# Kernel tuning notes

Hardware: AMD Instinct MI355X
Metric: run time of the kernel (lower is better)

The kernel has to match this reference:

```python
import jax, jax.numpy as jnp
import numpy as np

EMBED_DIM = 1024
NUM_HEADS = 16
HEAD_DIM = EMBED_DIM // NUM_HEADS


def setup_inputs() -> dict:
    key = jax.random.key(0)
    ks = jax.random.split(key, 9)
    B, T, D = 2, 4096, EMBED_DIM
    scale = 1.0 / np.sqrt(D)
    x = jax.random.normal(ks[0], (B, T, D), dtype=jnp.float32)
    # nn.Linear weights stored as (out, in); we use (in, out) layout via transpose-free init
    Wq = jax.random.uniform(ks[1], (D, D), dtype=jnp.float32, minval=-scale, maxval=scale)
    Wk = jax.random.uniform(ks[2], (D, D), dtype=jnp.float32, minval=-scale, maxval=scale)
    Wv = jax.random.uniform(ks[3], (D, D), dtype=jnp.float32, minval=-scale, maxval=scale)
    Wo = jax.random.uniform(ks[4], (D, D), dtype=jnp.float32, minval=-scale, maxval=scale)
    bq = jax.random.uniform(ks[5], (D,), dtype=jnp.float32, minval=-scale, maxval=scale)
    bk = jax.random.uniform(ks[6], (D,), dtype=jnp.float32, minval=-scale, maxval=scale)
    bv = jax.random.uniform(ks[7], (D,), dtype=jnp.float32, minval=-scale, maxval=scale)
    bo = jax.random.uniform(ks[8], (D,), dtype=jnp.float32, minval=-scale, maxval=scale)
    return {"x": x, "Wq": Wq, "bq": bq, "Wk": Wk, "bk": bk,
            "Wv": Wv, "bv": bv, "Wo": Wo, "bo": bo}


def reference(x, Wq, bq, Wk, bk, Wv, bv, Wo, bo):
    B, T, D = x.shape
    H, Hd = NUM_HEADS, HEAD_DIM
    q = x @ Wq + bq  # [B,T,D]
    k = x @ Wk + bk
    v = x @ Wv + bv
    # [B,T,D] -> [B,H,T,Hd]
    q = q.reshape(B, T, H, Hd).transpose(0, 2, 1, 3)
    k = k.reshape(B, T, H, Hd).transpose(0, 2, 1, 3)
    v = v.reshape(B, T, H, Hd).transpose(0, 2, 1, 3)
    att = jnp.einsum('bhqd,bhkd->bhqk', q, k) / jnp.sqrt(jnp.float32(Hd))
    causal = jnp.tril(jnp.ones((T, T), dtype=bool))  # True = keep
    att = jnp.where(causal, att, -jnp.inf)
    att = jax.nn.softmax(att, axis=-1)
    out = jnp.einsum('bhqk,bhkd->bhqd', att, v)  # [B,H,T,Hd]
    out = out.transpose(0, 2, 1, 3).reshape(B, T, D)
    return out @ Wo + bo
```

## Files before the change

### kernel.cpp

```cpp
#include <hip/hip_runtime.h>
#include <hip/hip_bf16.h>
#include <math.h>

typedef __bf16 bf16;
typedef __attribute__((ext_vector_type(8))) __bf16 bf16x8;
typedef __attribute__((ext_vector_type(4))) __bf16 bf16x4;
typedef __attribute__((ext_vector_type(4))) short short4v;
typedef __attribute__((ext_vector_type(4))) float f32x4;

#define MFMA16(a,b,c)  __builtin_amdgcn_mfma_f32_16x16x32_bf16((a),(b),(c),0,0,0)
#define MFMAK16(a,b,c) __builtin_amdgcn_mfma_f32_16x16x16bf16_1k((a),(b),(c),0,0,0)

__device__ __forceinline__ void gload16(const void* gp, void* lp) {
  __builtin_amdgcn_global_load_lds(
      (const __attribute__((address_space(1))) void*)gp,
      (__attribute__((address_space(3))) void*)lp, 16, 0, 0);
}

__global__ __launch_bounds__(256) void cast_x(
    const float* __restrict__ x, bf16* __restrict__ xb)
{
  size_t i = ((size_t)blockIdx.x*256 + threadIdx.x) * 8;
  f32x4 a = *(const f32x4*)(x+i);
  f32x4 b = *(const f32x4*)(x+i+4);
  bf16x8 o;
  #pragma unroll
  for (int j=0;j<4;j++) { o[j] = (bf16)a[j]; o[4+j] = (bf16)b[j]; }
  *(bf16x8*)(xb+i) = o;
}

__global__ __launch_bounds__(1024) void tr_cast(
    const float* __restrict__ w0, const float* __restrict__ w1,
    const float* __restrict__ w2, bf16* __restrict__ dst)
{
  __shared__ bf16 tile[64][65];
  const float* src = (blockIdx.z==0)?w0:(blockIdx.z==1)?w1:w2;
  bf16* d = dst + (size_t)blockIdx.z * (1024*1024);
  int x = threadIdx.x, y = threadIdx.y;
  int tc = blockIdx.x, tr = blockIdx.y;
  #pragma unroll
  for (int i=0;i<4;i++) {
    int r = y + i*16;
    tile[r][x] = (bf16)src[(size_t)(tr*64+r)*1024 + tc*64 + x];
  }
  __syncthreads();
  #pragma unroll
  for (int i=0;i<4;i++) {
    int r = y + i*16;
    d[(size_t)(tc*64+r)*1024 + tr*64 + x] = tile[x][r];
  }
}

__global__ __launch_bounds__(256) void gemm_qkv(
    const bf16* __restrict__ A, const bf16* __restrict__ Bt,
    const float* __restrict__ bq, const float* __restrict__ bk, const float* __restrict__ bv,
    bf16* __restrict__ q, bf16* __restrict__ k, bf16* __restrict__ v,
    int M, int K)
{
  __shared__ __align__(16) bf16 As[128*32];
  __shared__ __align__(16) bf16 Bs[128*32];
  const int tid  = threadIdx.x;
  const int wave = tid >> 6;
  const int lane = tid & 63;
  const int l15  = lane & 15;
  const int quad = lane >> 4;
  const int m0 = blockIdx.y * 128;
  const int n0 = blockIdx.x * 128;
  const int wm = (wave >> 1) * 64;
  const int wn = (wave & 1) * 64;
  const int srow = lane >> 2;
  const int scol = (lane & 3) * 8;

  f32x4 acc[4][4];
  #pragma unroll
  for (int i=0;i<4;i++)
    #pragma unroll
    for (int j=0;j<4;j++)
      acc[i][j] = (f32x4){0.f,0.f,0.f,0.f};

  for (int k0 = 0; k0 < K; k0 += 32) {
    __syncthreads();
    #pragma unroll
    for (int p=0;p<2;p++) {
      int c = p*4 + wave;
      int row = c*16 + srow;
      gload16(A  + (size_t)(m0+row)*K + k0 + scol, As + c*512);
      gload16(Bt + (size_t)(n0+row)*K + k0 + scol, Bs + c*512);
    }
    __syncthreads();
    bf16x8 af[4], bfr[4];
    #pragma unroll
    for (int t=0;t<4;t++) {
      af[t]  = *(const bf16x8*)(As + (wm + t*16 + l15)*32 + quad*8);
      bfr[t] = *(const bf16x8*)(Bs + (wn + t*16 + l15)*32 + quad*8);
    }
    #pragma unroll
    for (int mt=0;mt<4;mt++)
      #pragma unroll
      for (int nt=0;nt<4;nt++)
        acc[mt][nt] = MFMA16(af[mt], bfr[nt], acc[mt][nt]);
  }

  const int mat = n0 >> 10;
  const float* bsel = (mat==0) ? bq : (mat==1) ? bk : bv;
  bf16*       osel  = (mat==0) ? q  : (mat==1) ? k  : v;
  const float qsc   = (mat==0) ? 0.1803368801f : 1.0f;
  #pragma unroll
  for (int nt=0;nt<4;nt++) {
    int col = n0 + wn + nt*16 + l15;
    int cw  = col & 1023;
    float bvv = bsel[cw];
    #pragma unroll
    for (int mt=0;mt<4;mt++) {
      int row = m0 + wm + mt*16 + quad*4;
      #pragma unroll
      for (int r=0;r<4;r++)
        osel[(size_t)(row + r)*1024 + cw] = (bf16)((acc[mt][nt][r] + bvv) * qsc);
    }
  }
}

__global__ __launch_bounds__(256) void gemm_out(
    const bf16* __restrict__ A, const bf16* __restrict__ Bt,
    const float* __restrict__ bias, float* __restrict__ C,
    int M, int N, int K)
{
  __shared__ __align__(16) bf16 As[128*32];
  __shared__ __align__(16) bf16 Bs[128*32];
  const int tid  = threadIdx.x;
  const int wave = tid >> 6;
  const int lane = tid & 63;
  const int l15  = lane & 15;
  const int quad = lane >> 4;
  const int m0 = blockIdx.y * 128;
  const int n0 = blockIdx.x * 128;
  const int wm = (wave >> 1) * 64;
  const int wn = (wave & 1) * 64;
  const int srow = lane >> 2;
  const int scol = (lane & 3) * 8;

  f32x4 acc[4][4];
  #pragma unroll
  for (int i=0;i<4;i++)
    #pragma unroll
    for (int j=0;j<4;j++)
      acc[i][j] = (f32x4){0.f,0.f,0.f,0.f};

  for (int k0 = 0; k0 < K; k0 += 32) {
    __syncthreads();
    #pragma unroll
    for (int p=0;p<2;p++) {
      int c = p*4 + wave;
      int row = c*16 + srow;
      gload16(A  + (size_t)(m0+row)*K + k0 + scol, As + c*512);
      gload16(Bt + (size_t)(n0+row)*K + k0 + scol, Bs + c*512);
    }
    __syncthreads();
    bf16x8 af[4], bfr[4];
    #pragma unroll
    for (int t=0;t<4;t++) {
      af[t]  = *(const bf16x8*)(As + (wm + t*16 + l15)*32 + quad*8);
      bfr[t] = *(const bf16x8*)(Bs + (wn + t*16 + l15)*32 + quad*8);
    }
    #pragma unroll
    for (int mt=0;mt<4;mt++)
      #pragma unroll
      for (int nt=0;nt<4;nt++)
        acc[mt][nt] = MFMA16(af[mt], bfr[nt], acc[mt][nt]);
  }

  #pragma unroll
  for (int nt=0;nt<4;nt++) {
    int col = n0 + wn + nt*16 + l15;
    float bvv = bias[col];
    #pragma unroll
    for (int mt=0;mt<4;mt++) {
      int row = m0 + wm + mt*16 + quad*4;
      #pragma unroll
      for (int r=0;r<4;r++)
        C[(size_t)(row + r)*N + col] = acc[mt][nt][r] + bvv;
    }
  }
}

__global__ __launch_bounds__(256, 5) void attn_fwd(
    const bf16* __restrict__ Q, const bf16* __restrict__ Kp,
    const bf16* __restrict__ V, bf16* __restrict__ O)
{
  __shared__ __align__(16) char KsB[2*8192];
  __shared__ __align__(16) char VtB[2*8192];

  const int tid  = threadIdx.x;
  const int w    = tid >> 6;
  const int lane = tid & 63;
  const int l15  = lane & 15;
  const int quad = lane >> 4;

  const int bid = blockIdx.x;
  const int qt  = 63 - (bid >> 5);
  const int bh  = bid & 31;
  const int h   = bh & 15;
  const int b   = bh >> 4;

  const size_t headoff = (size_t)h * 64;
  const size_t bbase   = (size_t)b * 4096;

  bf16x8 aq[2];
  {
    int row = qt*64 + w*16 + l15;
    const bf16* qp = Q + (bbase + row)*1024 + headoff + quad*8;
    aq[0] = *(const bf16x8*)(qp);
    aq[1] = *(const bf16x8*)(qp + 32);
  }

  short4v ones_s;
  {
    bf16x4 o1;
    #pragma unroll
    for (int j=0;j<4;j++) o1[j] = (bf16)1.0f;
    ones_s = __builtin_bit_cast(short4v, o1);
  }

  f32x4 acco[4];
  f32x4 accli;
  #pragma unroll
  for (int i=0;i<4;i++) acco[i] = (f32x4){0.f,0.f,0.f,0.f};
  accli = (f32x4){0.f,0.f,0.f,0.f};

  const int kt_row = tid >> 2;
  const int kswz   = (kt_row & 7) << 4;
  const int ks_w0  = kt_row*128 + (((tid & 3)*32)      ^ kswz);
  const int ks_w1  = kt_row*128 + (((tid & 3)*32 + 16) ^ kswz);
  const int vt_wbase = w*2048;
  const int vt_wlane = 2*lane;

  const int s7    = l15 & 7;
  const int ks_r0 = l15*128 + ((quad ^ (s7 & 3)) << 4) + ((s7 >> 2) << 6);
  const int ks_r1 = ks_r0 ^ 64;
  const int vt_rbase = l15*128 + ((quad ^ (l15 & 3)) << 3) + ((l15 >> 2) << 5);
  int vt_r[4];
  #pragma unroll
  for (int tt=0;tt<4;tt++) vt_r[tt] = vt_rbase ^ (tt << 5);

  {
    const bf16* kp = Kp + (bbase + kt_row)*1024 + headoff + (tid & 3)*16;
    bf16x8 k0 = *(const bf16x8*)(kp);
    bf16x8 k1 = *(const bf16x8*)(kp + 8);
    *(bf16x8*)(KsB + ks_w0) = k0;
    *(bf16x8*)(KsB + ks_w1) = k1;
    const bf16* vp = V + (bbase + lane)*1024 + headoff + w*16;
    bf16x8 v0 = *(const bf16x8*)(vp);
    bf16x8 v1 = *(const bf16x8*)(vp + 8);
    #pragma unroll
    for (int j=0;j<8;j++) {
      *(bf16*)(VtB + vt_wbase + j*128     + (vt_wlane ^ (j<<3)))     = v0[j];
      *(bf16*)(VtB + vt_wbase + (8+j)*128 + (vt_wlane ^ ((8+j)<<3))) = v1[j];
    }
  }
  __syncthreads();

  const bf16* kpref = Kp + (bbase + 64 + kt_row)*1024 + headoff + (tid & 3)*16;
  const bf16* vpref = V  + (bbase + 64 + lane)*1024 + headoff + w*16;

  for (int kt = 0; kt <= qt; ++kt) {
    const int p = kt & 1;
    const bool pre = (kt < qt);

    bf16x8 kr0, kr1, vr0, vr1;
    if (pre) {
      kr0 = *(const bf16x8*)(kpref);
      kr1 = *(const bf16x8*)(kpref + 8);
      vr0 = *(const bf16x8*)(vpref);
      vr1 = *(const bf16x8*)(vpref + 8);
      kpref += 64*1024;
      vpref += 64*1024;
    }

    const char* ksb = KsB + p*8192;
    const char* vtb = VtB + p*8192;

    f32x4 accs[4];
    #pragma unroll
    for (int i=0;i<4;i++) accs[i] = (f32x4){0.f,0.f,0.f,0.f};

    __builtin_amdgcn_s_setprio(1);
    #pragma unroll
    for (int kk=0;kk<2;kk++) {
      #pragma unroll
      for (int tt=0;tt<4;tt++) {
        bf16x8 ka = *(const bf16x8*)(ksb + (kk ? ks_r1 : ks_r0) + tt*2048);
        accs[tt] = MFMA16(ka, aq[kk], accs[tt]);
      }
    }
    __builtin_amdgcn_s_setprio(0);

    const bool diag = (kt == qt);
    short4v pts[4];
    #pragma unroll
    for (int tt=0;tt<4;tt++) {
      bf16x4 pb;
      #pragma unroll
      for (int r=0;r<4;r++) {
        float tv = fminf(accs[tt][r], 60.0f);
        float pf = __builtin_amdgcn_exp2f(tv);
        if (diag && (tt*16 + quad*4 + r > w*16 + l15)) pf = 0.0f;
        pb[r] = (bf16)pf;
      }
      pts[tt] = __builtin_bit_cast(short4v, pb);
    }

    __builtin_amdgcn_s_setprio(1);
    #pragma unroll
    for (int nt=0;nt<4;nt++) {
      #pragma unroll
      for (int tt=0;tt<4;tt++) {
        bf16x4 va = *(const bf16x4*)(vtb + vt_r[tt] + nt*2048);
        acco[nt] = MFMAK16(__builtin_bit_cast(short4v, va), pts[tt], acco[nt]);
      }
    }
    #pragma unroll
    for (int tt=0;tt<4;tt++)
      accli = MFMAK16(ones_s, pts[tt], accli);
    __builtin_amdgcn_s_setprio(0);

    if (pre) {
      char* ksn = KsB + (p^1)*8192;
      char* vtn = VtB + (p^1)*8192;
      *(bf16x8*)(ksn + ks_w0) = kr0;
      *(bf16x8*)(ksn + ks_w1) = kr1;
      #pragma unroll
      for (int j=0;j<8;j++) {
        *(bf16*)(vtn + vt_wbase + j*128     + (vt_wlane ^ (j<<3)))     = vr0[j];
        *(bf16*)(vtn + vt_wbase + (8+j)*128 + (vt_wlane ^ ((8+j)<<3))) = vr1[j];
      }
      __syncthreads();
    }
  }

  {
    float inv = 1.0f / accli[0];
    int qrow = qt*64 + w*16 + l15;
    bf16* ob = O + (bbase + qrow)*1024 + headoff;
    #pragma unroll
    for (int nt=0;nt<4;nt++) {
      bf16x4 o;
      #pragma unroll
      for (int r=0;r<4;r++) o[r] = (bf16)(acco[nt][r] * inv);
      *(bf16x4*)(ob + nt*16 + quad*4) = o;
    }
  }
}

extern "C" void kernel_launch(void* const* d_in, const int* in_sizes, int n_in,
                              void* d_out, int out_size, void* d_ws, size_t ws_size,
                              hipStream_t stream) {
  const float* x  = (const float*)d_in[0];
  const float* Wq = (const float*)d_in[1];
  const float* bq = (const float*)d_in[2];
  const float* Wk = (const float*)d_in[3];
  const float* bk = (const float*)d_in[4];
  const float* Wv = (const float*)d_in[5];
  const float* bv = (const float*)d_in[6];
  const float* Wo = (const float*)d_in[7];
  const float* bo = (const float*)d_in[8];
  float* out = (float*)d_out;

  bf16* ws = (bf16*)d_ws;
  bf16* q  = ws;
  bf16* k  = q + (size_t)8192*1024;
  bf16* v  = k + (size_t)8192*1024;
  bf16* xb = v + (size_t)8192*1024;
  bf16* ao = q;
  bf16* WtQKV = (bf16*)d_out;
  bf16* WtO   = xb;

  tr_cast<<<dim3(16,16,3), dim3(64,16), 0, stream>>>(Wq, Wk, Wv, WtQKV);
  cast_x<<<4096, 256, 0, stream>>>(x, xb);
  gemm_qkv<<<dim3(24,64), 256, 0, stream>>>(xb, WtQKV, bq, bk, bv, q, k, v, 8192, 1024);
  tr_cast<<<dim3(16,16,1), dim3(64,16), 0, stream>>>(Wo, Wo, Wo, WtO);
  attn_fwd<<<2048, 256, 0, stream>>>(q, k, v, ao);
  gemm_out<<<dim3(8,64), 256, 0, stream>>>(ao, WtO, bo, out, 8192, 1024, 1024);
}
```

Baseline: 340.8 us.

## Write V pre-transposed from QKV GEMM so attention loads it with vector LDS stores

The QKV projection epilogue now writes V in a per-head transposed layout [B,H,Hd,T], storing contiguous bf16x4 along T. The attention kernel then reads V rows already transposed and writes them into the swizzled LDS tile with four 8-byte stores, replacing sixteen scalar 2-byte scattered stores per tile. This cuts LDS write instructions and bank traffic in the attention inner loop. The cost is a strided epilogue store in the GEMM, plus a change to the V layout contract between the two kernels.

```diff
diff --git a/kernel.cpp b/kernel.cpp
--- a/kernel.cpp
+++ b/kernel.cpp
@@ -102,20 +102,38 @@
   }
 
   const int mat = n0 >> 10;
-  const float* bsel = (mat==0) ? bq : (mat==1) ? bk : bv;
-  bf16*       osel  = (mat==0) ? q  : (mat==1) ? k  : v;
-  const float qsc   = (mat==0) ? 0.1803368801f : 1.0f;
-  #pragma unroll
-  for (int nt=0;nt<4;nt++) {
-    int col = n0 + wn + nt*16 + l15;
-    int cw  = col & 1023;
-    float bvv = bsel[cw];
-    #pragma unroll
-    for (int mt=0;mt<4;mt++) {
-      int row = m0 + wm + mt*16 + quad*4;
-      #pragma unroll
-      for (int r=0;r<4;r++)
-        osel[(size_t)(row + r)*1024 + cw] = (bf16)((acc[mt][nt][r] + bvv) * qsc);
+  if (mat == 2) {
+    #pragma unroll
+    for (int nt=0;nt<4;nt++) {
+      int col = (n0 & 1023) + wn + nt*16 + l15;
+      int hh = col >> 6, dl = col & 63;
+      float bvv = bv[col];
+      #pragma unroll
+      for (int mt=0;mt<4;mt++) {
+        int row = m0 + wm + mt*16 + quad*4;
+        int bb = row >> 12, tt = row & 4095;
+        bf16x4 o;
+        #pragma unroll
+        for (int r=0;r<4;r++) o[r] = (bf16)(acc[mt][nt][r] + bvv);
+        *(bf16x4*)(v + ((size_t)((bb*16 + hh)*64 + dl))*4096 + tt) = o;
+      }
+    }
+  } else {
+    const float* bsel = (mat==0) ? bq : bk;
+    bf16*       osel  = (mat==0) ? q  : k;
+    const float qsc   = (mat==0) ? 0.1803368801f : 1.0f;
+    #pragma unroll
+    for (int nt=0;nt<4;nt++) {
+      int col = n0 + wn + nt*16 + l15;
+      int cw  = col & 1023;
+      float bvv = bsel[cw];
+      #pragma unroll
+      for (int mt=0;mt<4;mt++) {
+        int row = m0 + wm + mt*16 + quad*4;
+        #pragma unroll
+        for (int r=0;r<4;r++)
+          osel[(size_t)(row + r)*1024 + cw] = (bf16)((acc[mt][nt][r] + bvv) * qsc);
+      }
     }
   }
 }
@@ -185,7 +203,7 @@
 
 __global__ __launch_bounds__(256, 5) void attn_fwd(
     const bf16* __restrict__ Q, const bf16* __restrict__ Kp,
-    const bf16* __restrict__ V, bf16* __restrict__ O)
+    const bf16* __restrict__ Vt, bf16* __restrict__ O)
 {
   __shared__ __align__(16) char KsB[2*8192];
   __shared__ __align__(16) char VtB[2*8192];
@@ -231,8 +249,14 @@
   const int kswz   = (kt_row & 7) << 4;
   const int ks_w0  = kt_row*128 + (((tid & 3)*32)      ^ kswz);
   const int ks_w1  = kt_row*128 + (((tid & 3)*32 + 16) ^ kswz);
-  const int vt_wbase = w*2048;
-  const int vt_wlane = 2*lane;
+
+  const int vd  = tid >> 2;
+  const int vt0 = (tid & 3) * 16;
+  int vw[4];
+  #pragma unroll
+  for (int u=0;u<4;u++)
+    vw[u] = vd*128 + (((vt0 + u*4)*2) ^ ((vd & 15) << 3));
+  const bf16* vbase = Vt + ((size_t)(b*16 + h) * 64 + vd) * 4096 + vt0;
 
   const int s7    = l15 & 7;
   const int ks_r0 = l15*128 + ((quad ^ (s7 & 3)) << 4) + ((s7 >> 2) << 6);
@@ -248,19 +272,17 @@
     bf16x8 k1 = *(const bf16x8*)(kp + 8);
     *(bf16x8*)(KsB + ks_w0) = k0;
     *(bf16x8*)(KsB + ks_w1) = k1;
-    const bf16* vp = V + (bbase + lane)*1024 + headoff + w*16;
-    bf16x8 v0 = *(const bf16x8*)(vp);
-    bf16x8 v1 = *(const bf16x8*)(vp + 8);
-    #pragma unroll
-    for (int j=0;j<8;j++) {
-      *(bf16*)(VtB + vt_wbase + j*128     + (vt_wlane ^ (j<<3)))     = v0[j];
-      *(bf16*)(VtB + vt_wbase + (8+j)*128 + (vt_wlane ^ ((8+j)<<3))) = v1[j];
-    }
+    bf16x8 v0 = *(const bf16x8*)(vbase);
+    bf16x8 v1 = *(const bf16x8*)(vbase + 8);
+    *(bf16x4*)(VtB + vw[0]) = __builtin_shufflevector(v0, v0, 0,1,2,3);
+    *(bf16x4*)(VtB + vw[1]) = __builtin_shufflevector(v0, v0, 4,5,6,7);
+    *(bf16x4*)(VtB + vw[2]) = __builtin_shufflevector(v1, v1, 0,1,2,3);
+    *(bf16x4*)(VtB + vw[3]) = __builtin_shufflevector(v1, v1, 4,5,6,7);
   }
   __syncthreads();
 
   const bf16* kpref = Kp + (bbase + 64 + kt_row)*1024 + headoff + (tid & 3)*16;
-  const bf16* vpref = V  + (bbase + 64 + lane)*1024 + headoff + w*16;
+  const bf16* vpref = vbase + 64;
 
   for (int kt = 0; kt <= qt; ++kt) {
     const int p = kt & 1;
@@ -273,7 +295,7 @@
       vr0 = *(const bf16x8*)(vpref);
       vr1 = *(const bf16x8*)(vpref + 8);
       kpref += 64*1024;
-      vpref += 64*1024;
+      vpref += 64;
     }
 
     const char* ksb = KsB + p*8192;
@@ -328,11 +350,10 @@
       char* vtn = VtB + (p^1)*8192;
       *(bf16x8*)(ksn + ks_w0) = kr0;
       *(bf16x8*)(ksn + ks_w1) = kr1;
-      #pragma unroll
-      for (int j=0;j<8;j++) {
-        *(bf16*)(vtn + vt_wbase + j*128     + (vt_wlane ^ (j<<3)))     = vr0[j];
-        *(bf16*)(vtn + vt_wbase + (8+j)*128 + (vt_wlane ^ ((8+j)<<3))) = vr1[j];
-      }
+      *(bf16x4*)(vtn + vw[0]) = __builtin_shufflevector(vr0, vr0, 0,1,2,3);
+      *(bf16x4*)(vtn + vw[1]) = __builtin_shufflevector(vr0, vr0, 4,5,6,7);
+      *(bf16x4*)(vtn + vw[2]) = __builtin_shufflevector(vr1, vr1, 0,1,2,3);
+      *(bf16x4*)(vtn + vw[3]) = __builtin_shufflevector(vr1, vr1, 4,5,6,7);
       __syncthreads();
     }
   }
```

Result: no change. 334.7 us (-1.8%).

## Process two query tiles per attention block with pre-transposed V and async LDS loads

Applied to the files above, without the earlier changes.

Each attention block now handles 128 query rows as two 64-row sub-tiles that share every K/V tile loaded into LDS, which halves K/V traffic per query. A new kernel transposes V into a per-head layout, so K and V^T tiles can be fetched straight into LDS with global_load_lds instead of going through registers and scattered per-element transposed stores. Query tiles are ordered in a snake pattern to balance the causal workload. The costs are one extra kernel launch and pass over V, twice the accumulator registers (occupancy hint drops from 5 to 4), and a wasted masked iteration for the first sub-tile on the last step.

```diff
diff --git a/kernel.cpp b/kernel.cpp
--- a/kernel.cpp
+++ b/kernel.cpp
@@ -48,6 +48,29 @@
   for (int i=0;i<4;i++) {
     int r = y + i*16;
     d[(size_t)(tc*64+r)*1024 + tr*64 + x] = tile[x][r];
+  }
+}
+
+__global__ __launch_bounds__(1024) void v_tr(
+    const bf16* __restrict__ v, bf16* __restrict__ vt)
+{
+  __shared__ bf16 tile[64][65];
+  int x = threadIdx.x, y = threadIdx.y;
+  int tt = blockIdx.x;
+  int bh = blockIdx.y;
+  int b = bh >> 4, h = bh & 15;
+  const bf16* src = v + ((size_t)b*4096 + tt*64)*1024 + h*64;
+  bf16* dst = vt + ((size_t)bh*64)*4096 + tt*64;
+  #pragma unroll
+  for (int i=0;i<4;i++) {
+    int r = y + i*16;
+    tile[r][x] = src[(size_t)r*1024 + x];
+  }
+  __syncthreads();
+  #pragma unroll
+  for (int i=0;i<4;i++) {
+    int r = y + i*16;
+    dst[(size_t)r*4096 + x] = tile[x][r];
   }
 }
 
@@ -183,9 +206,9 @@
   }
 }
 
-__global__ __launch_bounds__(256, 5) void attn_fwd(
+__global__ __launch_bounds__(256, 4) void attn_fwd(
     const bf16* __restrict__ Q, const bf16* __restrict__ Kp,
-    const bf16* __restrict__ V, bf16* __restrict__ O)
+    const bf16* __restrict__ Vtg, bf16* __restrict__ O)
 {
   __shared__ __align__(16) char KsB[2*8192];
   __shared__ __align__(16) char VtB[2*8192];
@@ -197,20 +220,26 @@
   const int quad = lane >> 4;
 
   const int bid = blockIdx.x;
-  const int qt  = 63 - (bid >> 5);
-  const int bh  = bid & 31;
-  const int h   = bh & 15;
-  const int b   = bh >> 4;
+  const int g  = bid >> 5;
+  const int u  = g >> 3, vv = g & 7;
+  const int qt = 8*u + ((u & 1) ? (7 - vv) : vv);
+  const int bh = bid & 31;
+  const int h  = bh & 15;
+  const int b  = bh >> 4;
 
   const size_t headoff = (size_t)h * 64;
   const size_t bbase   = (size_t)b * 4096;
-
-  bf16x8 aq[2];
+  const int q0 = qt * 128;
+
+  bf16x8 aqA[2], aqB[2];
   {
-    int row = qt*64 + w*16 + l15;
-    const bf16* qp = Q + (bbase + row)*1024 + headoff + quad*8;
-    aq[0] = *(const bf16x8*)(qp);
-    aq[1] = *(const bf16x8*)(qp + 32);
+    int rowA = q0 + w*16 + l15;
+    const bf16* qp = Q + (bbase + rowA)*1024 + headoff + quad*8;
+    aqA[0] = *(const bf16x8*)(qp);
+    aqA[1] = *(const bf16x8*)(qp + 32);
+    qp += 64*1024;
+    aqB[0] = *(const bf16x8*)(qp);
+    aqB[1] = *(const bf16x8*)(qp + 32);
   }
 
   short4v ones_s;
@@ -221,67 +250,52 @@
     ones_s = __builtin_bit_cast(short4v, o1);
   }
 
-  f32x4 acco[4];
-  f32x4 accli;
-  #pragma unroll
-  for (int i=0;i<4;i++) acco[i] = (f32x4){0.f,0.f,0.f,0.f};
-  accli = (f32x4){0.f,0.f,0.f,0.f};
-
-  const int kt_row = tid >> 2;
-  const int kswz   = (kt_row & 7) << 4;
-  const int ks_w0  = kt_row*128 + (((tid & 3)*32)      ^ kswz);
-  const int ks_w1  = kt_row*128 + (((tid & 3)*32 + 16) ^ kswz);
-  const int vt_wbase = w*2048;
-  const int vt_wlane = 2*lane;
+  f32x4 accoA[4], accoB[4], accliA, accliB;
+  #pragma unroll
+  for (int i=0;i<4;i++) { accoA[i] = (f32x4){0.f,0.f,0.f,0.f}; accoB[i] = (f32x4){0.f,0.f,0.f,0.f}; }
+  accliA = (f32x4){0.f,0.f,0.f,0.f};
+  accliB = (f32x4){0.f,0.f,0.f,0.f};
+
+  const int lrow = 16*w + (lane >> 3);
+  const int lcol = ((lane & 7) ^ (lane >> 3)) * 8;
+  const bf16* kgp = Kp  + (bbase + lrow)*1024 + headoff + lcol;
+  const bf16* vgp = Vtg + ((size_t)(bh*64) + lrow)*4096 + lcol;
+  char* const kb0 = KsB + w*2048;
+  char* const vb0 = VtB + w*2048;
 
   const int s7    = l15 & 7;
   const int ks_r0 = l15*128 + ((quad ^ (s7 & 3)) << 4) + ((s7 >> 2) << 6);
   const int ks_r1 = ks_r0 ^ 64;
-  const int vt_rbase = l15*128 + ((quad ^ (l15 & 3)) << 3) + ((l15 >> 2) << 5);
-  int vt_r[4];
-  #pragma unroll
-  for (int tt=0;tt<4;tt++) vt_r[tt] = vt_rbase ^ (tt << 5);
-
-  {
-    const bf16* kp = Kp + (bbase + kt_row)*1024 + headoff + (tid & 3)*16;
-    bf16x8 k0 = *(const bf16x8*)(kp);
-    bf16x8 k1 = *(const bf16x8*)(kp + 8);
-    *(bf16x8*)(KsB + ks_w0) = k0;
-    *(bf16x8*)(KsB + ks_w1) = k1;
-    const bf16* vp = V + (bbase + lane)*1024 + headoff + w*16;
-    bf16x8 v0 = *(const bf16x8*)(vp);
-    bf16x8 v1 = *(const bf16x8*)(vp + 8);
-    #pragma unroll
-    for (int j=0;j<8;j++) {
-      *(bf16*)(VtB + vt_wbase + j*128     + (vt_wlane ^ (j<<3)))     = v0[j];
-      *(bf16*)(VtB + vt_wbase + (8+j)*128 + (vt_wlane ^ ((8+j)<<3))) = v1[j];
-    }
-  }
+  const int vt_rb = l15*128 + ((quad << 3) ^ (s7 << 4));
+
+  gload16(kgp,            kb0);
+  gload16(kgp + 8*1024,   kb0 + 1024);
+  gload16(vgp,            vb0);
+  gload16(vgp + 8*4096,   vb0 + 1024);
   __syncthreads();
-
-  const bf16* kpref = Kp + (bbase + 64 + kt_row)*1024 + headoff + (tid & 3)*16;
-  const bf16* vpref = V  + (bbase + 64 + lane)*1024 + headoff + w*16;
-
-  for (int kt = 0; kt <= qt; ++kt) {
+  kgp += 64*1024;
+  vgp += 64;
+
+  const int ktmax = 2*qt + 1;
+  for (int kt = 0; kt <= ktmax; ++kt) {
     const int p = kt & 1;
-    const bool pre = (kt < qt);
-
-    bf16x8 kr0, kr1, vr0, vr1;
-    if (pre) {
-      kr0 = *(const bf16x8*)(kpref);
-      kr1 = *(const bf16x8*)(kpref + 8);
-      vr0 = *(const bf16x8*)(vpref);
-      vr1 = *(const bf16x8*)(vpref + 8);
-      kpref += 64*1024;
-      vpref += 64*1024;
+    if (kt < ktmax) {
+      char* kb = KsB + (p^1)*8192 + w*2048;
+      char* vb = VtB + (p^1)*8192 + w*2048;
+      gload16(kgp,          kb);
+      gload16(kgp + 8*1024, kb + 1024);
+      gload16(vgp,          vb);
+      gload16(vgp + 8*4096, vb + 1024);
+      kgp += 64*1024;
+      vgp += 64;
     }
 
     const char* ksb = KsB + p*8192;
     const char* vtb = VtB + p*8192;
 
-    f32x4 accs[4];
-    #pragma unroll
-    for (int i=0;i<4;i++) accs[i] = (f32x4){0.f,0.f,0.f,0.f};
+    f32x4 accsA[4], accsB[4];
+    #pragma unroll
+    for (int i=0;i<4;i++) { accsA[i] = (f32x4){0.f,0.f,0.f,0.f}; accsB[i] = (f32x4){0.f,0.f,0.f,0.f}; }
 
     __builtin_amdgcn_s_setprio(1);
     #pragma unroll
@@ -289,24 +303,30 @@
       #pragma unroll
       for (int tt=0;tt<4;tt++) {
         bf16x8 ka = *(const bf16x8*)(ksb + (kk ? ks_r1 : ks_r0) + tt*2048);
-        accs[tt] = MFMA16(ka, aq[kk], accs[tt]);
+        accsA[tt] = MFMA16(ka, aqA[kk], accsA[tt]);
+        accsB[tt] = MFMA16(ka, aqB[kk], accsB[tt]);
       }
     }
     __builtin_amdgcn_s_setprio(0);
 
-    const bool diag = (kt == qt);
-    short4v pts[4];
+    const bool Adiag = (kt == 2*qt);
+    const bool Adead = (kt >  2*qt);
+    const bool Bdiag = (kt == ktmax);
+    short4v ptsA[4], ptsB[4];
     #pragma unroll
     for (int tt=0;tt<4;tt++) {
-      bf16x4 pb;
+      bf16x4 pa, pb;
       #pragma unroll
       for (int r=0;r<4;r++) {
-        float tv = fminf(accs[tt][r], 60.0f);
-        float pf = __builtin_amdgcn_exp2f(tv);
-        if (diag && (tt*16 + quad*4 + r > w*16 + l15)) pf = 0.0f;
-        pb[r] = (bf16)pf;
+        const bool tq = (tt*16 + quad*4 + r > w*16 + l15);
+        float fa = __builtin_amdgcn_exp2f(fminf(accsA[tt][r], 60.0f));
+        if (Adead || (Adiag && tq)) fa = 0.0f;
+        float fb = __builtin_amdgcn_exp2f(fminf(accsB[tt][r], 60.0f));
+        if (Bdiag && tq) fb = 0.0f;
+        pa[r] = (bf16)fa; pb[r] = (bf16)fb;
       }
-      pts[tt] = __builtin_bit_cast(short4v, pb);
+      ptsA[tt] = __builtin_bit_cast(short4v, pa);
+      ptsB[tt] = __builtin_bit_cast(short4v, pb);
     }
 
     __builtin_amdgcn_s_setprio(1);
@@ -314,39 +334,38 @@
     for (int nt=0;nt<4;nt++) {
       #pragma unroll
       for (int tt=0;tt<4;tt++) {
-        bf16x4 va = *(const bf16x4*)(vtb + vt_r[tt] + nt*2048);
-        acco[nt] = MFMAK16(__builtin_bit_cast(short4v, va), pts[tt], acco[nt]);
+        bf16x4 va = *(const bf16x4*)(vtb + (vt_rb ^ (tt<<5)) + nt*2048);
+        short4v vas = __builtin_bit_cast(short4v, va);
+        accoA[nt] = MFMAK16(vas, ptsA[tt], accoA[nt]);
+        accoB[nt] = MFMAK16(vas, ptsB[tt], accoB[nt]);
       }
     }
     #pragma unroll
-    for (int tt=0;tt<4;tt++)
-      accli = MFMAK16(ones_s, pts[tt], accli);
+    for (int tt=0;tt<4;tt++) {
+      accliA = MFMAK16(ones_s, ptsA[tt], accliA);
+      accliB = MFMAK16(ones_s, ptsB[tt], accliB);
+    }
     __builtin_amdgcn_s_setprio(0);
 
-    if (pre) {
-      char* ksn = KsB + (p^1)*8192;
-      char* vtn = VtB + (p^1)*8192;
-      *(bf16x8*)(ksn + ks_w0) = kr0;
-      *(bf16x8*)(ksn + ks_w1) = kr1;
-      #pragma unroll
-      for (int j=0;j<8;j++) {
-        *(bf16*)(vtn + vt_wbase + j*128     + (vt_wlane ^ (j<<3)))     = vr0[j];
-        *(bf16*)(vtn + vt_wbase + (8+j)*128 + (vt_wlane ^ ((8+j)<<3))) = vr1[j];
+    __syncthreads();
+  }
+
+  {
+    float invA = 1.0f / accliA[0];
+    float invB = 1.0f / accliB[0];
+    int rowA = q0 + w*16 + l15;
+    bf16* obA = O + (bbase + rowA)*1024 + headoff;
+    bf16* obB = obA + 64*1024;
+    #pragma unroll
+    for (int nt=0;nt<4;nt++) {
+      bf16x4 oA, oB;
+      #pragma unroll
+      for (int r=0;r<4;r++) {
+        oA[r] = (bf16)(accoA[nt][r] * invA);
+        oB[r] = (bf16)(accoB[nt][r] * invB);
       }
-      __syncthreads();
-    }
-  }
-
-  {
-    float inv = 1.0f / accli[0];
-    int qrow = qt*64 + w*16 + l15;
-    bf16* ob = O + (bbase + qrow)*1024 + headoff;
-    #pragma unroll
-    for (int nt=0;nt<4;nt++) {
-      bf16x4 o;
-      #pragma unroll
-      for (int r=0;r<4;r++) o[r] = (bf16)(acco[nt][r] * inv);
-      *(bf16x4*)(ob + nt*16 + quad*4) = o;
+      *(bf16x4*)(obA + nt*16 + quad*4) = oA;
+      *(bf16x4*)(obB + nt*16 + quad*4) = oB;
     }
   }
 }
@@ -372,12 +391,14 @@
   bf16* xb = v + (size_t)8192*1024;
   bf16* ao = q;
   bf16* WtQKV = (bf16*)d_out;
+  bf16* vT    = (bf16*)d_out;
   bf16* WtO   = xb;
 
   tr_cast<<<dim3(16,16,3), dim3(64,16), 0, stream>>>(Wq, Wk, Wv, WtQKV);
   cast_x<<<4096, 256, 0, stream>>>(x, xb);
   gemm_qkv<<<dim3(24,64), 256, 0, stream>>>(xb, WtQKV, bq, bk, bv, q, k, v, 8192, 1024);
+  v_tr<<<dim3(64,32), dim3(64,16), 0, stream>>>(v, vT);
   tr_cast<<<dim3(16,16,1), dim3(64,16), 0, stream>>>(Wo, Wo, Wo, WtO);
-  attn_fwd<<<2048, 256, 0, stream>>>(q, k, v, ao);
+  attn_fwd<<<1024, 256, 0, stream>>>(q, k, vT, ao);
   gemm_out<<<dim3(8,64), 256, 0, stream>>>(ao, WtO, bo, out, 8192, 1024, 1024);
 }
```

Measured after the change: 342.1 us. About the same (+0.4%).
